# Kernel tuning notes

Hardware: AMD Instinct MI355X
Metric: run time of the kernel (lower is better)

Reference implementation:

```python
import jax, jax.numpy as jnp
import numpy as np

DIM = 2048       # model dim
HID = 1024       # expert hidden dim
E = 8            # num_experts
K = 2            # top_k
SHID = HID * 1   # shared expert hidden = hidden_dim * num_shared_experts
INIT = 0.02


def setup_inputs() -> dict:
    key = jax.random.key(0)
    ks = jax.random.split(key, 9)
    return {
        "x": jax.random.normal(ks[0], (2, 1024, DIM), jnp.float32),
        "expert_bias": jnp.zeros((E,), jnp.float32),
        "gate_w": jax.random.normal(ks[1], (E, DIM), jnp.float32) * INIT,
        "w1": jax.random.normal(ks[2], (E, HID, DIM), jnp.float32) * INIT,
        "w2": jax.random.normal(ks[3], (E, DIM, HID), jnp.float32) * INIT,
        "w3": jax.random.normal(ks[4], (E, HID, DIM), jnp.float32) * INIT,
        "sw1": jax.random.normal(ks[5], (SHID, DIM), jnp.float32) * INIT,
        "sw2": jax.random.normal(ks[6], (DIM, SHID), jnp.float32) * INIT,
        "sw3": jax.random.normal(ks[7], (SHID, DIM), jnp.float32) * INIT,
    }


def reference(x, expert_bias, gate_w, w1, w2, w3, sw1, sw2, sw3):
    B, S, D = x.shape
    xf = x.reshape(-1, D)                      # [N, D]
    N = xf.shape[0]

    # --- TokenChoiceTopKRouter (sigmoid score, bias-adjusted top-k selection) ---
    scores = jax.nn.sigmoid((xf @ gate_w.T).astype(jnp.float32))      # [N, E]
    _, sel = jax.lax.top_k(scores + expert_bias[None, :], K)          # [N, K] indices
    top_scores = jnp.take_along_axis(scores, sel, axis=1)             # [N, K] (route_norm=False, route_scale=1.0)

    # --- TokenReorderer: stable sort routed slots by expert id ---
    flat_exp = sel.reshape(-1)                                        # [N*K]
    order = jnp.argsort(flat_exp, stable=True)                        # expert-sorted slot order
    sorted_exp = flat_exp[order]                                      # [N*K]
    tok_idx = order // K                                              # source token per slot
    sc_sorted = top_scores.reshape(-1)[order]                         # [N*K]

    # score_before_experts=True: scale input by routing score before expert FFN
    rin = xf[tok_idx] * sc_sorted[:, None].astype(x.dtype)            # [N*K, D]

    # --- GroupedExperts: per-expert SwiGLU on the expert-sorted token block ---
    # (grouped GEMM expressed as a masked loop over the fixed expert set)
    out_sorted = jnp.zeros_like(rin)
    for e in range(E):
        m = (sorted_exp == e)[:, None].astype(rin.dtype)
        h = jax.nn.silu(rin @ w1[e].T) * (rin @ w3[e].T)              # [N*K, HID]
        out_sorted = out_sorted + m * (h @ w2[e].T)

    # combine: scatter-add expert outputs back to tokens
    routed = jnp.zeros((N, D), x.dtype).at[tok_idx].add(out_sorted)

    # shared expert (plain SwiGLU FeedForward)
    shared = (jax.nn.silu(xf @ sw1.T) * (xf @ sw3.T)) @ sw2.T

    return (routed + shared).reshape(B, S, D)
```

## Files before the change

### kernel.cpp

```cpp
#include <hip/hip_runtime.h>
#include <hip/hip_bf16.h>
#include <stdint.h>

#define DIMM 2048
#define HIDD 1024
#define NEXP 8
#define TOPK 2
#define NTOK 2048
#define CAP_E 1024
#define SH_BASE (NEXP * CAP_E)
#define NROW (SH_BASE + NTOK)

typedef __bf16 bf16_t;
typedef __bf16 bf16x4 __attribute__((ext_vector_type(4)));
typedef __bf16 bf16x8 __attribute__((ext_vector_type(8)));
typedef float f32x4 __attribute__((ext_vector_type(4)));

__device__ __forceinline__ void gl2lds16(const bf16_t* g, bf16_t* l) {
    __builtin_amdgcn_global_load_lds(
        (const __attribute__((address_space(1))) void*)g,
        (__attribute__((address_space(3))) void*)l, 16, 0, 0);
}

__global__ __launch_bounds__(256) void router_k(const float* __restrict__ x,
                                                const float* __restrict__ gw,
                                                const float* __restrict__ bias,
                                                int* __restrict__ sel,
                                                float* __restrict__ topsc) {
    int t = blockIdx.x;
    int tid = threadIdx.x;
    const float* xr = x + (long)t * DIMM;
    double acc[NEXP];
#pragma unroll
    for (int e = 0; e < NEXP; ++e) acc[e] = 0.0;
    for (int d = tid; d < DIMM; d += 256) {
        double xv = (double)xr[d];
#pragma unroll
        for (int e = 0; e < NEXP; ++e) acc[e] += xv * (double)gw[e * DIMM + d];
    }
#pragma unroll
    for (int off = 32; off >= 1; off >>= 1)
#pragma unroll
        for (int e = 0; e < NEXP; ++e) acc[e] += __shfl_down(acc[e], off, 64);
    __shared__ double red[4][NEXP];
    int lane = tid & 63, w = tid >> 6;
    if (lane == 0)
#pragma unroll
        for (int e = 0; e < NEXP; ++e) red[w][e] = acc[e];
    __syncthreads();
    if (tid == 0) {
        double sc[NEXP], v[NEXP];
#pragma unroll
        for (int e = 0; e < NEXP; ++e) {
            double s = red[0][e] + red[1][e] + red[2][e] + red[3][e];
            sc[e] = 1.0 / (1.0 + exp(-s));
            v[e] = sc[e] + (double)bias[e];
        }
        int b0 = 0;
        for (int e = 1; e < NEXP; ++e) if (v[e] > v[b0]) b0 = e;
        int b1 = -1;
        for (int e = 0; e < NEXP; ++e)
            if (e != b0 && (b1 < 0 || v[e] > v[b1])) b1 = e;
        sel[t * 2] = b0; sel[t * 2 + 1] = b1;
        topsc[t * 2] = (float)sc[b0]; topsc[t * 2 + 1] = (float)sc[b1];
    }
}

__global__ __launch_bounds__(256) void sort_k(const int* __restrict__ sel,
                                              const float* __restrict__ topsc,
                                              int* __restrict__ tok_s,
                                              float* __restrict__ sc_s,
                                              int* __restrict__ counts,
                                              int* __restrict__ pos) {
    __shared__ int se[NTOK * TOPK];
    int tid = threadIdx.x;
    for (int i = tid; i < NTOK * TOPK; i += 256) se[i] = sel[i];
    __syncthreads();
    int wv = tid >> 6, lane = tid & 63;
    unsigned long long lower = (1ull << lane) - 1ull;
    for (int ei = 0; ei < 2; ++ei) {
        int e = wv * 2 + ei;
        int base = e * CAP_E;
        int off = 0;
        for (int c = 0; c < (NTOK * TOPK) / 64; ++c) {
            int slot = c * 64 + lane;
            bool m = (se[slot] == e);
            unsigned long long bal = __ballot(m);
            if (m) {
                int rank = off + __popcll(bal & lower);
                if (rank < CAP_E) {
                    tok_s[base + rank] = slot >> 1;
                    sc_s[base + rank] = topsc[slot];
                    pos[slot] = base + rank;
                } else {
                    pos[slot] = -1;
                }
            }
            off += __popcll(bal);
        }
        int cnt = min(off, CAP_E);
        if (lane == 0) counts[e] = cnt;
        int padded = min((cnt + 127) & ~127, CAP_E);
        for (int r = cnt + lane; r < padded; r += 64) tok_s[base + r] = -1;
    }
}

__global__ __launch_bounds__(256) void build_rin(const float* __restrict__ x,
                                                 const int* __restrict__ tok_s,
                                                 const float* __restrict__ sc_s,
                                                 const int* __restrict__ counts,
                                                 bf16_t* __restrict__ rin) {
    int row = blockIdx.x;
    int tok; float sc = 1.0f;
    if (row >= SH_BASE) {
        tok = row - SH_BASE;
    } else {
        int e = row >> 10, r = row & (CAP_E - 1);
        int cnt = min(counts[e], CAP_E);
        int padded = min((cnt + 127) & ~127, CAP_E);
        if (r >= padded) return;
        if (r < cnt) { tok = tok_s[row]; sc = sc_s[row]; }
        else tok = -1;
    }
    int d0 = threadIdx.x * 8;
    bf16x8 o;
    if (tok >= 0) {
        const float* src = x + (long)tok * DIMM + d0;
        float4 a = *(const float4*)src;
        float4 b = *(const float4*)(src + 4);
        o[0] = (bf16_t)(a.x * sc); o[1] = (bf16_t)(a.y * sc);
        o[2] = (bf16_t)(a.z * sc); o[3] = (bf16_t)(a.w * sc);
        o[4] = (bf16_t)(b.x * sc); o[5] = (bf16_t)(b.y * sc);
        o[6] = (bf16_t)(b.z * sc); o[7] = (bf16_t)(b.w * sc);
    } else {
#pragma unroll
        for (int i = 0; i < 8; ++i) o[i] = (bf16_t)0.0f;
    }
    *(bf16x8*)(rin + (long)row * DIMM + d0) = o;
}


#define STAGE_A(kt, buf) do { \
    _Pragma("unroll") \
    for (int i_ = 0; i_ < 4; ++i_) \
        gl2lds16(arow[i_] + (kt) * 64, &lA[buf][(i_ * 256 + tid) * 8]); \
} while (0)

#define LOAD_B(kt, s) do { \
    _Pragma("unroll") \
    for (int i_ = 0; i_ < 4; ++i_) { \
        const float* bp_ = brow[i_] + (kt) * 64; \
        u##s[i_] = *(const float4*)bp_; \
        v##s[i_] = *(const float4*)(bp_ + 4); \
    } \
} while (0)

#define WRITE_B(s, buf) do { \
    _Pragma("unroll") \
    for (int i_ = 0; i_ < 4; ++i_) { \
        bf16x8 o_ = {(bf16_t)u##s[i_].x, (bf16_t)u##s[i_].y, \
                     (bf16_t)u##s[i_].z, (bf16_t)u##s[i_].w, \
                     (bf16_t)v##s[i_].x, (bf16_t)v##s[i_].y, \
                     (bf16_t)v##s[i_].z, (bf16_t)v##s[i_].w}; \
        *(bf16x8*)&lB[buf][slot[i_] * 8] = o_; \
    } \
} while (0)

#define MFMA_TILE(buf) do { \
    _Pragma("unroll") \
    for (int ki_ = 0; ki_ < 2; ++ki_) { \
        bf16x8 af_[4], bg_[4]; \
        int kc_ = ki_ * 4 + quad; \
        _Pragma("unroll") \
        for (int mi_ = 0; mi_ < 4; ++mi_) { \
            int row_ = wm + mi_ * 16 + l16; \
            af_[mi_] = *(const bf16x8*)&lA[buf][(row_ * 8 + (kc_ ^ (row_ & 7))) * 8]; \
        } \
        _Pragma("unroll") \
        for (int ni_ = 0; ni_ < 4; ++ni_) { \
            int row_ = wn + ni_ * 16 + l16; \
            bg_[ni_] = *(const bf16x8*)&lB[buf][(row_ * 8 + (kc_ ^ (row_ & 7))) * 8]; \
        } \
        _Pragma("unroll") \
        for (int mi_ = 0; mi_ < 4; ++mi_) \
            _Pragma("unroll") \
            for (int ni_ = 0; ni_ < 4; ++ni_) \
                acc[mi_][ni_] = __builtin_amdgcn_mfma_f32_16x16x32_bf16( \
                    af_[mi_], bg_[ni_], acc[mi_][ni_], 0, 0, 0); \
    } \
} while (0)

template <int PHASE>
__global__ __launch_bounds__(256, 2) void gemm_moe(
    const bf16_t* __restrict__ A0,
    const float* __restrict__ W1, const float* __restrict__ W3,
    const float* __restrict__ SW1, const float* __restrict__ SW3,
    bf16_t* __restrict__ hOut, float* __restrict__ C2,
    const int* __restrict__ counts) {
    constexpr int K = (PHASE == 1) ? 2048 : 1024;
    constexpr int KT = K / 64;
    int g = blockIdx.z;
    int base = (g < 8) ? g * CAP_E : SH_BASE;
    int M = NTOK;
    if (g < 8) {
        int c = min(counts[g], CAP_E);
        M = min((c + 127) & ~127, CAP_E);
    }
    int m0 = blockIdx.y * 128;
    if (m0 >= M) return;
    const bf16_t* A = A0 + (long)base * K;

    __shared__ bf16_t lA[2][128 * 64];
    __shared__ bf16_t lB[2][128 * 64];

    int tid = threadIdx.x;
    int lane = tid & 63, wv = tid >> 6;
    int quad = lane >> 4, l16 = lane & 15;
    int wm = (wv & 1) * 64, wn = (wv >> 1) * 64;
    int cc = tid & 7;
    int rbase = tid >> 3;

    const bf16_t* arow[4];
#pragma unroll
    for (int i = 0; i < 4; ++i) {
        int row = i * 32 + rbase;
        arow[i] = A + (long)(m0 + row) * K + (cc ^ (row & 7)) * 8;
    }
    const float* brow[4];
    int slot[4];
#pragma unroll
    for (int i = 0; i < 4; ++i) {
        int r = i * 32 + rbase;
        const float* p;
        if (PHASE == 1) {
            int colw = (blockIdx.x << 6) + ((r >> 5) << 4) + (r & 15);
            int type = (r >> 4) & 1;
            if (g < 8) p = (type ? W3 : W1) + ((long)g << 21) + (long)colw * DIMM;
            else       p = (type ? SW3 : SW1) + (long)colw * DIMM;
        } else {
            int n = (blockIdx.x << 7) + r;
            p = ((g < 8) ? W1 + ((long)g << 21) : SW1) + (long)n * HIDD;
        }
        brow[i] = p + cc * 8;
        slot[i] = r * 8 + (cc ^ (r & 7));
    }

    f32x4 acc[4][4];
#pragma unroll
    for (int i = 0; i < 4; ++i)
#pragma unroll
        for (int j = 0; j < 4; ++j) acc[i][j] = (f32x4){0.f, 0.f, 0.f, 0.f};

    float4 u0[4], v0[4], u1[4], v1[4];
    STAGE_A(0, 0);
    LOAD_B(0, 0);
    WRITE_B(0, 0);
    LOAD_B(1, 1);
    __syncthreads();

    for (int kt = 0; kt < KT; kt += 2) {
        STAGE_A(kt + 1, 1);
        if (kt + 2 < KT) LOAD_B(kt + 2, 0);
        MFMA_TILE(0);
        WRITE_B(1, 1);
        __syncthreads();
        if (kt + 2 < KT) {
            STAGE_A(kt + 2, 0);
            if (kt + 3 < KT) LOAD_B(kt + 3, 1);
        }
        MFMA_TILE(1);
        if (kt + 2 < KT) WRITE_B(0, 0);
        __syncthreads();
    }

    if (PHASE == 1) {
#pragma unroll
        for (int mi = 0; mi < 4; ++mi)
#pragma unroll
            for (int r = 0; r < 4; ++r) {
                long row = base + m0 + wm + mi * 16 + quad * 4 + r;
#pragma unroll
                for (int j = 0; j < 2; ++j) {
                    float gt = acc[mi][2 * j][r];
                    float up = acc[mi][2 * j + 1][r];
                    float s = gt / (1.f + __expf(-gt));
                    int col = (blockIdx.x << 6) + ((wn >> 5) + j) * 16 + l16;
                    hOut[row * HIDD + col] = (bf16_t)(s * up);
                }
            }
    } else {
#pragma unroll
        for (int mi = 0; mi < 4; ++mi)
#pragma unroll
            for (int r = 0; r < 4; ++r) {
                long row = base + m0 + wm + mi * 16 + quad * 4 + r;
#pragma unroll
                for (int ni = 0; ni < 4; ++ni) {
                    int col = (blockIdx.x << 7) + wn + ni * 16 + l16;
                    C2[row * DIMM + col] = acc[mi][ni][r];
                }
            }
    }
}

__global__ __launch_bounds__(256) void combine_k(const float* __restrict__ C2,
                                                 const int* __restrict__ pos,
                                                 float* __restrict__ out) {
    int t = blockIdx.x;
    int c = threadIdx.x * 8;
    int p0 = pos[t * 2], p1 = pos[t * 2 + 1];
    const float* sh = C2 + (long)(SH_BASE + t) * DIMM + c;
    float4 a = *(const float4*)sh;
    float4 b = *(const float4*)(sh + 4);
    if (p0 >= 0) {
        const float* q = C2 + (long)p0 * DIMM + c;
        float4 qa = *(const float4*)q, qb = *(const float4*)(q + 4);
        a.x += qa.x; a.y += qa.y; a.z += qa.z; a.w += qa.w;
        b.x += qb.x; b.y += qb.y; b.z += qb.z; b.w += qb.w;
    }
    if (p1 >= 0) {
        const float* q = C2 + (long)p1 * DIMM + c;
        float4 qa = *(const float4*)q, qb = *(const float4*)(q + 4);
        a.x += qa.x; a.y += qa.y; a.z += qa.z; a.w += qa.w;
        b.x += qb.x; b.y += qb.y; b.z += qb.z; b.w += qb.w;
    }
    float* op = out + (long)t * DIMM + c;
    *(float4*)op = a;
    *(float4*)(op + 4) = b;
}

extern "C" void kernel_launch(void* const* d_in, const int* in_sizes, int n_in,
                              void* d_out, int out_size, void* d_ws, size_t ws_size,
                              hipStream_t stream) {
    const float* x    = (const float*)d_in[0];
    const float* bias = (const float*)d_in[1];
    const float* gw   = (const float*)d_in[2];
    const float* w1   = (const float*)d_in[3];
    const float* w2   = (const float*)d_in[4];
    const float* w3   = (const float*)d_in[5];
    const float* sw1  = (const float*)d_in[6];
    const float* sw2  = (const float*)d_in[7];
    const float* sw3  = (const float*)d_in[8];
    float* out = (float*)d_out;

    char* p = (char*)d_ws;
    auto alloc = [&](size_t bytes) {
        char* r = p;
        p += (bytes + 255) & ~(size_t)255;
        return r;
    };
    bf16_t* rin   = (bf16_t*)alloc((size_t)NROW * DIMM * 2);
    bf16_t* hB    = (bf16_t*)alloc((size_t)NROW * HIDD * 2);
    float*  C2    = (float*)alloc((size_t)NROW * DIMM * 4);
    int*   sel    = (int*)alloc(NTOK * TOPK * 4);
    float* topsc  = (float*)alloc(NTOK * TOPK * 4);
    int*   tok_s  = (int*)alloc(SH_BASE * 4);
    float* sc_s   = (float*)alloc(SH_BASE * 4);
    int*   pos    = (int*)alloc(NTOK * TOPK * 4);
    int*   counts = (int*)alloc(256);

    router_k<<<NTOK, 256, 0, stream>>>(x, gw, bias, sel, topsc);
    sort_k<<<1, 256, 0, stream>>>(sel, topsc, tok_s, sc_s, counts, pos);
    build_rin<<<NROW, 256, 0, stream>>>(x, tok_s, sc_s, counts, rin);

    gemm_moe<1><<<dim3(16, 16, 9), 256, 0, stream>>>(
        rin, w1, w3, sw1, sw3, hB, nullptr, counts);

    gemm_moe<2><<<dim3(16, 16, 9), 256, 0, stream>>>(
        hB, w2, nullptr, sw2, nullptr, nullptr, C2, counts);

    combine_k<<<NTOK, 256, 0, stream>>>(C2, pos, out);
}
```

Before: 416.2 us.

## Fuse combine into down-proj GEMM via atomic scatter-add; register-stage A loads

Removes the fp32 C2 intermediate and the separate combine kernel: the second GEMM phase now atomically adds its outputs straight into the zeroed output rows, indexed through tok_s, and build_rin zeroes the output. The A operand path also changes from direct global-to-LDS loads to register-staged loads written to LDS together with B, with an unswizzled global address. This saves writing and re-reading a large fp32 buffer and one launch. In exchange it adds many fp32 atomics, makes the summation order nondeterministic, and loses the async LDS loads for A.

```diff
diff --git a/kernel.cpp b/kernel.cpp
--- a/kernel.cpp
+++ b/kernel.cpp
@@ -15,12 +15,6 @@
 typedef __bf16 bf16x4 __attribute__((ext_vector_type(4)));
 typedef __bf16 bf16x8 __attribute__((ext_vector_type(8)));
 typedef float f32x4 __attribute__((ext_vector_type(4)));
-
-__device__ __forceinline__ void gl2lds16(const bf16_t* g, bf16_t* l) {
-    __builtin_amdgcn_global_load_lds(
-        (const __attribute__((address_space(1))) void*)g,
-        (__attribute__((address_space(3))) void*)l, 16, 0, 0);
-}
 
 __global__ __launch_bounds__(256) void router_k(const float* __restrict__ x,
                                                 const float* __restrict__ gw,
@@ -70,8 +64,7 @@
                                               const float* __restrict__ topsc,
                                               int* __restrict__ tok_s,
                                               float* __restrict__ sc_s,
-                                              int* __restrict__ counts,
-                                              int* __restrict__ pos) {
+                                              int* __restrict__ counts) {
     __shared__ int se[NTOK * TOPK];
     int tid = threadIdx.x;
     for (int i = tid; i < NTOK * TOPK; i += 256) se[i] = sel[i];
@@ -91,9 +84,6 @@
                 if (rank < CAP_E) {
                     tok_s[base + rank] = slot >> 1;
                     sc_s[base + rank] = topsc[slot];
-                    pos[slot] = base + rank;
-                } else {
-                    pos[slot] = -1;
                 }
             }
             off += __popcll(bal);
@@ -109,8 +99,13 @@
                                                  const int* __restrict__ tok_s,
                                                  const float* __restrict__ sc_s,
                                                  const int* __restrict__ counts,
-                                                 bf16_t* __restrict__ rin) {
+                                                 bf16_t* __restrict__ rin,
+                                                 float* __restrict__ outz) {
     int row = blockIdx.x;
+    int tid = threadIdx.x;
+    if (row < 4096)
+        ((f32x4*)outz)[row * 256 + tid] = (f32x4){0.f, 0.f, 0.f, 0.f};
+
     int tok; float sc = 1.0f;
     if (row >= SH_BASE) {
         tok = row - SH_BASE;
@@ -122,7 +117,7 @@
         if (r < cnt) { tok = tok_s[row]; sc = sc_s[row]; }
         else tok = -1;
     }
-    int d0 = threadIdx.x * 8;
+    int d0 = tid * 8;
     bf16x8 o;
     if (tok >= 0) {
         const float* src = x + (long)tok * DIMM + d0;
@@ -140,24 +135,20 @@
 }
 
 
-#define STAGE_A(kt, buf) do { \
-    _Pragma("unroll") \
-    for (int i_ = 0; i_ < 4; ++i_) \
-        gl2lds16(arow[i_] + (kt) * 64, &lA[buf][(i_ * 256 + tid) * 8]); \
-} while (0)
-
-#define LOAD_B(kt, s) do { \
+#define LOADAB(kt, s) do { \
     _Pragma("unroll") \
     for (int i_ = 0; i_ < 4; ++i_) { \
+        a##s[i_] = *(const bf16x8*)(arow[i_] + (kt) * 64); \
         const float* bp_ = brow[i_] + (kt) * 64; \
         u##s[i_] = *(const float4*)bp_; \
         v##s[i_] = *(const float4*)(bp_ + 4); \
     } \
 } while (0)
 
-#define WRITE_B(s, buf) do { \
+#define WRITEAB(s, buf) do { \
     _Pragma("unroll") \
     for (int i_ = 0; i_ < 4; ++i_) { \
+        *(bf16x8*)&lA[buf][slot[i_] * 8] = a##s[i_]; \
         bf16x8 o_ = {(bf16_t)u##s[i_].x, (bf16_t)u##s[i_].y, \
                      (bf16_t)u##s[i_].z, (bf16_t)u##s[i_].w, \
                      (bf16_t)v##s[i_].x, (bf16_t)v##s[i_].y, \
@@ -195,8 +186,8 @@
     const bf16_t* __restrict__ A0,
     const float* __restrict__ W1, const float* __restrict__ W3,
     const float* __restrict__ SW1, const float* __restrict__ SW3,
-    bf16_t* __restrict__ hOut, float* __restrict__ C2,
-    const int* __restrict__ counts) {
+    bf16_t* __restrict__ hOut, float* __restrict__ outp,
+    const int* __restrict__ counts, const int* __restrict__ tok_s) {
     constexpr int K = (PHASE == 1) ? 2048 : 1024;
     constexpr int KT = K / 64;
     int g = blockIdx.z;
@@ -221,16 +212,12 @@
     int rbase = tid >> 3;
 
     const bf16_t* arow[4];
-#pragma unroll
-    for (int i = 0; i < 4; ++i) {
-        int row = i * 32 + rbase;
-        arow[i] = A + (long)(m0 + row) * K + (cc ^ (row & 7)) * 8;
-    }
     const float* brow[4];
     int slot[4];
 #pragma unroll
     for (int i = 0; i < 4; ++i) {
         int r = i * 32 + rbase;
+        arow[i] = A + (long)(m0 + r) * K + cc * 8;
         const float* p;
         if (PHASE == 1) {
             int colw = (blockIdx.x << 6) + ((r >> 5) << 4) + (r & 15);
@@ -251,25 +238,22 @@
 #pragma unroll
         for (int j = 0; j < 4; ++j) acc[i][j] = (f32x4){0.f, 0.f, 0.f, 0.f};
 
+    bf16x8 a0[4], a1[4];
     float4 u0[4], v0[4], u1[4], v1[4];
-    STAGE_A(0, 0);
-    LOAD_B(0, 0);
-    WRITE_B(0, 0);
-    LOAD_B(1, 1);
+
+    LOADAB(0, 0);
+    LOADAB(1, 1);
+    WRITEAB(0, 0);
     __syncthreads();
 
     for (int kt = 0; kt < KT; kt += 2) {
-        STAGE_A(kt + 1, 1);
-        if (kt + 2 < KT) LOAD_B(kt + 2, 0);
+        if (kt + 2 < KT) LOADAB(kt + 2, 0);
+        WRITEAB(1, 1);
         MFMA_TILE(0);
-        WRITE_B(1, 1);
         __syncthreads();
-        if (kt + 2 < KT) {
-            STAGE_A(kt + 2, 0);
-            if (kt + 3 < KT) LOAD_B(kt + 3, 1);
-        }
+        if (kt + 3 < KT) LOADAB(kt + 3, 1);
+        if (kt + 2 < KT) WRITEAB(0, 0);
         MFMA_TILE(1);
-        if (kt + 2 < KT) WRITE_B(0, 0);
         __syncthreads();
     }
 
@@ -293,40 +277,16 @@
         for (int mi = 0; mi < 4; ++mi)
 #pragma unroll
             for (int r = 0; r < 4; ++r) {
-                long row = base + m0 + wm + mi * 16 + quad * 4 + r;
-#pragma unroll
-                for (int ni = 0; ni < 4; ++ni) {
-                    int col = (blockIdx.x << 7) + wn + ni * 16 + l16;
-                    C2[row * DIMM + col] = acc[mi][ni][r];
+                int rloc = m0 + wm + mi * 16 + quad * 4 + r;
+                int tok = (g < 8) ? tok_s[g * CAP_E + rloc] : rloc;
+                if (tok >= 0) {
+                    float* op = outp + (long)tok * DIMM + (blockIdx.x << 7) + wn + l16;
+#pragma unroll
+                    for (int ni = 0; ni < 4; ++ni)
+                        atomicAdd(op + ni * 16, acc[mi][ni][r]);
                 }
             }
     }
-}
-
-__global__ __launch_bounds__(256) void combine_k(const float* __restrict__ C2,
-                                                 const int* __restrict__ pos,
-                                                 float* __restrict__ out) {
-    int t = blockIdx.x;
-    int c = threadIdx.x * 8;
-    int p0 = pos[t * 2], p1 = pos[t * 2 + 1];
-    const float* sh = C2 + (long)(SH_BASE + t) * DIMM + c;
-    float4 a = *(const float4*)sh;
-    float4 b = *(const float4*)(sh + 4);
-    if (p0 >= 0) {
-        const float* q = C2 + (long)p0 * DIMM + c;
-        float4 qa = *(const float4*)q, qb = *(const float4*)(q + 4);
-        a.x += qa.x; a.y += qa.y; a.z += qa.z; a.w += qa.w;
-        b.x += qb.x; b.y += qb.y; b.z += qb.z; b.w += qb.w;
-    }
-    if (p1 >= 0) {
-        const float* q = C2 + (long)p1 * DIMM + c;
-        float4 qa = *(const float4*)q, qb = *(const float4*)(q + 4);
-        a.x += qa.x; a.y += qa.y; a.z += qa.z; a.w += qa.w;
-        b.x += qb.x; b.y += qb.y; b.z += qb.z; b.w += qb.w;
-    }
-    float* op = out + (long)t * DIMM + c;
-    *(float4*)op = a;
-    *(float4*)(op + 4) = b;
 }
 
 extern "C" void kernel_launch(void* const* d_in, const int* in_sizes, int n_in,
@@ -351,23 +311,19 @@
     };
     bf16_t* rin   = (bf16_t*)alloc((size_t)NROW * DIMM * 2);
     bf16_t* hB    = (bf16_t*)alloc((size_t)NROW * HIDD * 2);
-    float*  C2    = (float*)alloc((size_t)NROW * DIMM * 4);
     int*   sel    = (int*)alloc(NTOK * TOPK * 4);
     float* topsc  = (float*)alloc(NTOK * TOPK * 4);
     int*   tok_s  = (int*)alloc(SH_BASE * 4);
     float* sc_s   = (float*)alloc(SH_BASE * 4);
-    int*   pos    = (int*)alloc(NTOK * TOPK * 4);
     int*   counts = (int*)alloc(256);
 
     router_k<<<NTOK, 256, 0, stream>>>(x, gw, bias, sel, topsc);
-    sort_k<<<1, 256, 0, stream>>>(sel, topsc, tok_s, sc_s, counts, pos);
-    build_rin<<<NROW, 256, 0, stream>>>(x, tok_s, sc_s, counts, rin);
+    sort_k<<<1, 256, 0, stream>>>(sel, topsc, tok_s, sc_s, counts);
+    build_rin<<<NROW, 256, 0, stream>>>(x, tok_s, sc_s, counts, rin, out);
 
     gemm_moe<1><<<dim3(16, 16, 9), 256, 0, stream>>>(
-        rin, w1, w3, sw1, sw3, hB, nullptr, counts);
+        rin, w1, w3, sw1, sw3, hB, nullptr, counts, nullptr);
 
     gemm_moe<2><<<dim3(16, 16, 9), 256, 0, stream>>>(
-        hB, w2, nullptr, sw2, nullptr, nullptr, C2, counts);
-
-    combine_k<<<NTOK, 256, 0, stream>>>(C2, pos, out);
-}
+        hB, w2, nullptr, sw2, nullptr, nullptr, out, counts, tok_s);
+}
```

Measured after the change: 494.5 us. +18.8%, slower.
